# Performance work log

Measured on AMD Instinct MI355X. Metric: run time of the kernel, lower is better.

## Reference

```python
import jax, jax.numpy as jnp
import numpy as np

EMBED_DIM = 512
NUM_HEADS = 8
HEAD_DIM = EMBED_DIM // NUM_HEADS  # 64
KERNEL = 3  # spatial neighborhood kernel (time kernel is full t)
EPS = 1e-6


def _rms_norm(u, gamma):
    # RMSNorm over the last (head_dim) axis
    return u * jax.lax.rsqrt(jnp.mean(u * u, axis=-1, keepdims=True) + EPS) * gamma


def _apply_rotary(x, freqs):
    # x: (b, t, h, w, nh, hd); freqs: (t, h, w, hd//2) angles
    cos = jnp.cos(freqs)[None, :, :, :, None, :]
    sin = jnp.sin(freqs)[None, :, :, :, None, :]
    xe, xo = x[..., 0::2], x[..., 1::2]
    out = jnp.stack([xe * cos - xo * sin, xe * sin + xo * cos], axis=-1)
    return out.reshape(x.shape)


def setup_inputs() -> dict:
    key = jax.random.key(0)
    ks = jax.random.split(key, 6)
    b, t, h, w = 2, 8, 32, 32
    x = jax.random.normal(ks[0], (b, t, h, w, EMBED_DIM), dtype=jnp.float32)
    freqs = jax.random.normal(ks[1], (t, h, w, HEAD_DIM // 2), dtype=jnp.float32)
    w_in = jax.random.normal(ks[2], (3 * EMBED_DIM, EMBED_DIM), dtype=jnp.float32) * 0.02
    w_out = jax.random.normal(ks[3], (EMBED_DIM, EMBED_DIM), dtype=jnp.float32) * 0.02
    q_gamma = jnp.ones((HEAD_DIM,), dtype=jnp.float32)
    k_gamma = jnp.ones((HEAD_DIM,), dtype=jnp.float32)
    return {"x": x, "freqs": freqs, "w_in": w_in, "w_out": w_out,
            "q_gamma": q_gamma, "k_gamma": k_gamma}


def reference(x, freqs, w_in, w_out, q_gamma, k_gamma):
    b, t, H, W, c = x.shape
    nh, hd = NUM_HEADS, HEAD_DIM
    # fused QKV projection (torch Linear: y = x @ W^T)
    qkv = jnp.einsum('bthwc,oc->bthwo', x, w_in).reshape(b, t, H, W, nh, 3 * hd)
    q, k, v = jnp.split(qkv, 3, axis=-1)
    q = _apply_rotary(_rms_norm(q, q_gamma), freqs)
    k = _apply_rotary(_rms_norm(k, k_gamma), freqs)
    # NATTEN 3D neighborhood: full attention over time, 3x3 spatial window
    # clamped to stay inside the feature map (window shifts near borders).
    Kc = KERNEL // 2
    ih = jnp.clip(jnp.arange(H) - Kc, 0, H - KERNEL)[:, None] + jnp.arange(KERNEL)  # (H,3)
    iw = jnp.clip(jnp.arange(W) - Kc, 0, W - KERNEL)[:, None] + jnp.arange(KERNEL)  # (W,3)

    def window(u):
        # u: (b, t, H, W, nh, hd) -> (b, H, W, nh, t*K*K, hd)
        uw = jnp.take(jnp.take(u, ih, axis=2), iw, axis=4)  # (b,t,H,K,W,K,nh,hd)
        uw = jnp.transpose(uw, (0, 2, 4, 6, 1, 3, 5, 7))     # (b,H,W,nh,t,K,K,hd)
        return uw.reshape(b, H, W, nh, t * KERNEL * KERNEL, hd)

    k_win = window(k)
    v_win = window(v)
    scale = hd ** -0.5
    scores = jnp.einsum('bthwnd,bhwnkd->bhwntk', q, k_win) * scale
    attn = jax.nn.softmax(scores, axis=-1)
    out = jnp.einsum('bhwntk,bhwnkd->bthwnd', attn, v_win)
    out = out.reshape(b, t, H, W, nh * hd)
    return jnp.einsum('bthwc,oc->bthwo', out, w_out)
```

## Files before the change

### kernel.cpp

```cpp
#include <hip/hip_runtime.h>
#include <hip/hip_bf16.h>
#include <math.h>

#define NH 8
#define C_ 512
#define C3 1536
#define NTOK 16384

typedef __attribute__((ext_vector_type(8))) short short8;
typedef __attribute__((ext_vector_type(4))) float f32x4;
typedef __attribute__((address_space(3))) void* lds_ptr_t;
typedef const __attribute__((address_space(1))) void* gbl_ptr_t;

static __device__ __forceinline__ ushort f2bf(float f) {
  __hip_bfloat16 h = __float2bfloat16(f);
  return *reinterpret_cast<ushort*>(&h);
}
static __device__ __forceinline__ float bf2f(ushort u) {
  uint t = ((uint)u) << 16;
  float f;
  __builtin_memcpy(&f, &t, 4);
  return f;
}

__global__ __launch_bounds__(256) void cast3_kernel(
    const float* __restrict__ x, const float* __restrict__ wi,
    const float* __restrict__ wo, ushort* __restrict__ xb,
    ushort* __restrict__ wib, ushort* __restrict__ wob) {
  const int blk = blockIdx.x;
  const float* src;
  ushort* dst;
  int i;
  if (blk < 4096)      { src = x;  dst = xb;  i = blk * 256 + threadIdx.x; }
  else if (blk < 4480) { src = wi; dst = wib; i = (blk - 4096) * 256 + threadIdx.x; }
  else                 { src = wo; dst = wob; i = (blk - 4480) * 256 + threadIdx.x; }
  const float4* p = (const float4*)src + (size_t)i * 2;
  float4 v0 = p[0], v1 = p[1];
  union { ushort u[8]; uint4 v; } r;
  r.u[0] = f2bf(v0.x); r.u[1] = f2bf(v0.y); r.u[2] = f2bf(v0.z); r.u[3] = f2bf(v0.w);
  r.u[4] = f2bf(v1.x); r.u[5] = f2bf(v1.y); r.u[6] = f2bf(v1.z); r.u[7] = f2bf(v1.w);
  *(uint4*)(dst + (size_t)i * 8) = r.v;
}

#define TBM 128
#define TBN 128
#define TBK 32
#define TILE_U ((TBM + TBN) * TBK)

static __device__ __forceinline__ void stage_tile(
    const ushort* __restrict__ A, const ushort* __restrict__ B,
    ushort* As, ushort* Bs, int bm, int bn, int K, int k0, int tid) {
#pragma unroll
  for (int it = 0; it < 2; ++it) {
    int c = it * 256 + tid;
    int row = c >> 2;
    int sk = ((c & 3) ^ ((row >> 1) & 3)) * 8;
    __builtin_amdgcn_global_load_lds(
        (gbl_ptr_t)(const void*)(A + (size_t)(bm + row) * K + k0 + sk),
        (lds_ptr_t)(As + (size_t)c * 8), 16, 0, 0);
    __builtin_amdgcn_global_load_lds(
        (gbl_ptr_t)(const void*)(B + (size_t)(bn + row) * K + k0 + sk),
        (lds_ptr_t)(Bs + (size_t)c * 8), 16, 0, 0);
  }
}

template <bool BF16OUT>
__global__ __launch_bounds__(256) void gemm_bt_bf16(
    const ushort* __restrict__ A, const ushort* __restrict__ B,
    void* __restrict__ Cv, int N, int K, int GX) {
  __shared__ ushort smem[2 * TILE_U];
  const int tid  = threadIdx.x;
  const int wave = tid >> 6;
  const int lane = tid & 63;
  const int nwg = gridDim.x;
  const int wg = (blockIdx.x & 7) * (nwg >> 3) + (blockIdx.x >> 3);
  const int bm = (wg / GX) * TBM;
  const int bn = (wg % GX) * TBN;
  const int wr = (wave >> 1) * 64;
  const int wc = (wave & 1) * 64;
  const int lm = lane & 15;
  const int g4 = lane >> 4;

  f32x4 acc[4][4];
#pragma unroll
  for (int m = 0; m < 4; ++m)
#pragma unroll
    for (int n = 0; n < 4; ++n) acc[m][n] = (f32x4){0.f, 0.f, 0.f, 0.f};

  const int ko = (g4 ^ ((lm >> 1) & 3)) * 8;

  const int nt = K / TBK;
  stage_tile(A, B, smem, smem + TBM * TBK, bm, bn, K, 0, tid);
  __syncthreads();

  int cur = 0;
  for (int t = 0; t < nt; ++t) {
    if (t + 1 < nt) {
      ushort* Asn = smem + (cur ^ 1) * TILE_U;
      stage_tile(A, B, Asn, Asn + TBM * TBK, bm, bn, K, (t + 1) * TBK, tid);
    }
    const ushort* As = smem + cur * TILE_U;
    const ushort* Bs = As + TBM * TBK;
    short8 av[4], bv[4];
#pragma unroll
    for (int m = 0; m < 4; ++m)
      av[m] = *(const short8*)&As[(wr + m * 16 + lm) * TBK + ko];
#pragma unroll
    for (int n = 0; n < 4; ++n)
      bv[n] = *(const short8*)&Bs[(wc + n * 16 + lm) * TBK + ko];
#pragma unroll
    for (int m = 0; m < 4; ++m)
#pragma unroll
      for (int n = 0; n < 4; ++n)
        acc[m][n] = __builtin_amdgcn_mfma_f32_16x16x32_bf16(av[m], bv[n], acc[m][n], 0, 0, 0);
    __syncthreads();
    cur ^= 1;
  }

  const int cr = g4 * 4;
  const int cc = lm;

  if (BF16OUT) {
    ushort* Cs = smem;
    ushort* C = (ushort*)Cv;
#pragma unroll
    for (int h = 0; h < 2; ++h) {
      __syncthreads();
      if ((wave >> 1) == h) {
#pragma unroll
        for (int m = 0; m < 4; ++m)
#pragma unroll
          for (int n = 0; n < 4; ++n)
#pragma unroll
            for (int r = 0; r < 4; ++r)
              Cs[(m * 16 + cr + r) * 128 + wc + n * 16 + cc] = f2bf(acc[m][n][r]);
      }
      __syncthreads();
#pragma unroll
      for (int i = 0; i < 4; ++i) {
        int idx = i * 256 + tid;
        int row = idx >> 4, ch = idx & 15;
        uint4 v = *(const uint4*)&Cs[row * 128 + ch * 8];
        *(uint4*)(C + (size_t)(bm + h * 64 + row) * N + bn + ch * 8) = v;
      }
    }
  } else {
    float* Csf = (float*)smem;
    float* C = (float*)Cv;
#pragma unroll
    for (int s = 0; s < 4; ++s) {
      __syncthreads();
      if ((wave >> 1) == (s >> 1)) {
#pragma unroll
        for (int mi = 0; mi < 2; ++mi)
#pragma unroll
          for (int n = 0; n < 4; ++n)
#pragma unroll
            for (int r = 0; r < 4; ++r) {
              int m = (s & 1) * 2 + mi;
              Csf[(mi * 16 + cr + r) * 128 + wc + n * 16 + cc] = acc[m][n][r];
            }
      }
      __syncthreads();
#pragma unroll
      for (int i = 0; i < 4; ++i) {
        int idx = i * 256 + tid;
        int row = idx >> 5, ch = idx & 31;
        float4 v = *(const float4*)&Csf[row * 128 + ch * 4];
        *(float4*)(C + (size_t)(bm + s * 32 + row) * N + bn + ch * 4) = v;
      }
    }
  }
}

__global__ __launch_bounds__(256) void norm_rope_kernel(
    ushort* __restrict__ qkv, const float* __restrict__ freqs,
    const float* __restrict__ qg, const float* __restrict__ kg) {
  const int task = blockIdx.x * 4 + (threadIdx.x >> 6);
  const int L = threadIdx.x & 63;
  const int n = task & 7;
  const int m = task >> 3;
  const int w = m & 31, h = (m >> 5) & 31, t = (m >> 10) & 7;
  const int dp = L & 31;

  ushort* base = qkv + (size_t)m * C3 + n * 192;
  uint val = *(uint*)(base + 2 * L);
  float x0 = bf2f((ushort)(val & 0xffffu));
  float x1 = bf2f((ushort)(val >> 16));

  float ss = x0 * x0 + x1 * x1;
#pragma unroll
  for (int off = 16; off >= 1; off >>= 1) ss += __shfl_xor(ss, off, 32);
  const float r = rsqrtf(ss * (1.f / 64.f) + 1e-6f);
  const float* gp = (L < 32) ? qg : kg;
  const float xe = x0 * r * gp[2 * dp];
  const float xo = x1 * r * gp[2 * dp + 1];

  const float f = freqs[(((t * 32 + h) * 32 + w) * 32) + dp];
  const float c = cosf(f), s = sinf(f);
  ushort o0 = f2bf(xe * c - xo * s);
  ushort o1 = f2bf(xe * s + xo * c);
  *(uint*)(base + 2 * L) = (uint)o0 | ((uint)o1 << 16);
}

__global__ __launch_bounds__(256) void attn_kernel(
    const ushort* __restrict__ qkv, ushort* __restrict__ outb) {
  __shared__ ushort lds[24576];
  ushort* K_s  = lds;
  ushort* Vt_s = lds + 12288;
  ushort* P_s  = lds;
  ushort* O_s  = lds + 12288;

  const int tid = threadIdx.x;
  const int wave = tid >> 6;
  const int lane = tid & 63;
  const int lin = blockIdx.x;
  const int bid = (lin & 7) * 256 + (lin >> 3);
  const int tw = bid & 7, th = (bid >> 3) & 15, n = (bid >> 7) & 7, b = bid >> 10;
  const int hb = th * 2, wb = tw * 4;
  const int hb0 = max(hb - 1, 0), wb0 = max(wb - 1, 0);
  const int lm = lane & 15, g4 = lane >> 4;

  float4 vreg[6];
#pragma unroll
  for (int it = 0; it < 6; ++it) {
    int c = it * 256 + tid;
    int kr = c >> 3, gv = c & 7;
    int sc = kr >> 3, t = kr & 7;
    int kh = sc / 6, kw = sc - kh * 6;
    int hh = min(hb0 + kh, 31), ww = min(wb0 + kw, 31);
    size_t m = (((size_t)(b * 8 + t) * 32 + hh) * 32 + ww);
    vreg[it] = *(const float4*)(qkv + m * C3 + n * 192 + 128 + gv * 8);
  }

#pragma unroll
  for (int it = 0; it < 6; ++it) {
    int c = it * 256 + tid;
    int kr = c >> 3, g = (c & 7) ^ (kr & 7);
    int sc = kr >> 3, t = kr & 7;
    int kh = sc / 6, kw = sc - kh * 6;
    int hh = min(hb0 + kh, 31), ww = min(wb0 + kw, 31);
    size_t m = (((size_t)(b * 8 + t) * 32 + hh) * 32 + ww);
    const ushort* srcK = qkv + m * C3 + n * 192 + 64 + g * 8;
    ushort* dstK = K_s + (size_t)(it * 256 + wave * 64) * 8;
    __builtin_amdgcn_global_load_lds((gbl_ptr_t)(const void*)srcK, (lds_ptr_t)dstK, 16, 0, 0);
  }

  short8 bq[2];
  {
    int q = wave * 16 + lm;
    int tq = q >> 3, p = q & 7;
    size_t mq = (((size_t)(b * 8 + tq) * 32 + (hb + (p >> 2))) * 32 + (wb + (p & 3)));
    const ushort* qp = qkv + mq * C3 + n * 192;
#pragma unroll
    for (int kk = 0; kk < 2; ++kk)
      bq[kk] = *(const short8*)(qp + (kk * 4 + g4) * 8);
  }

  __syncthreads();

#pragma unroll
  for (int it = 0; it < 6; ++it) {
    int c = it * 256 + tid;
    int kr = c >> 3, gv = c & 7;
    int ck = kr >> 3, kin = kr & 7;
    union { float4 f; ushort u[8]; } vv;
    vv.f = vreg[it];
#pragma unroll
    for (int j = 0; j < 8; ++j) {
      int d = gv * 8 + j;
      int cks = ck ^ ((j ^ gv) & 7);
      Vt_s[d * 192 + cks * 8 + kin] = vv.u[j];
    }
  }

  f32x4 st[12];
#pragma unroll
  for (int kf = 0; kf < 12; ++kf) st[kf] = (f32x4){0.f, 0.f, 0.f, 0.f};
#pragma unroll
  for (int kk = 0; kk < 2; ++kk)
#pragma unroll
    for (int kf = 0; kf < 12; ++kf) {
      int kr = kf * 16 + lm;
      short8 a = *(const short8*)&K_s[kr * 64 + (((kk * 4 + g4) ^ (kr & 7)) * 8)];
      st[kf] = __builtin_amdgcn_mfma_f32_16x16x32_bf16(a, bq[kk], st[kf], 0, 0, 0);
    }

  const int p = lm & 7;
  const int qh = hb + (p >> 2), qw = wb + (p & 3);
  const int loh = min(max(qh - 1, 0), 29), low = min(max(qw - 1, 0), 29);
  uint mk = 0;
#pragma unroll
  for (int kf = 0; kf < 12; ++kf) {
    int sc = kf * 2 + (g4 >> 1);
    int kh = sc / 6, kw = sc - kh * 6;
    int khg = hb0 + kh, kwg = wb0 + kw;
    bool ok = (khg >= loh) && (khg <= loh + 2) && (kwg >= low) && (kwg <= low + 2);
    mk |= (uint)ok << kf;
  }
  const float scale = 0.125f;
#pragma unroll
  for (int kf = 0; kf < 12; ++kf) {
    bool ok = (mk >> kf) & 1;
#pragma unroll
    for (int r = 0; r < 4; ++r)
      st[kf][r] = ok ? st[kf][r] * scale : -1e30f;
  }
  float mx = -1e30f;
#pragma unroll
  for (int kf = 0; kf < 12; ++kf)
#pragma unroll
    for (int r = 0; r < 4; ++r) mx = fmaxf(mx, st[kf][r]);
  mx = fmaxf(mx, __shfl_xor(mx, 16));
  mx = fmaxf(mx, __shfl_xor(mx, 32));
  float s = 0.f;
#pragma unroll
  for (int kf = 0; kf < 12; ++kf)
#pragma unroll
    for (int r = 0; r < 4; ++r) {
      float e = __expf(st[kf][r] - mx);
      st[kf][r] = e;
      s += e;
    }
  s += __shfl_xor(s, 16);
  s += __shfl_xor(s, 32);
  const float inv = 1.f / s;
  __syncthreads();

  {
    const int q = wave * 16 + lm;
    ushort* Prow = P_s + q * 192 + (g4 & 1) * 4;
#pragma unroll
    for (int kf = 0; kf < 12; ++kf) {
      uint lo = (uint)f2bf(st[kf][0] * inv) | ((uint)f2bf(st[kf][1] * inv) << 16);
      uint hi = (uint)f2bf(st[kf][2] * inv) | ((uint)f2bf(st[kf][3] * inv) << 16);
      int ck = kf * 2 + (g4 >> 1);
      int cks = ck ^ (lm & 7);
      uint2 val; val.x = lo; val.y = hi;
      *(uint2*)(Prow + cks * 8) = val;
    }
  }
  __syncthreads();

  f32x4 ao0 = (f32x4){0.f, 0.f, 0.f, 0.f};
  f32x4 ao1 = (f32x4){0.f, 0.f, 0.f, 0.f};
  f32x4 ao2 = (f32x4){0.f, 0.f, 0.f, 0.f};
  f32x4 ao3 = (f32x4){0.f, 0.f, 0.f, 0.f};
  const int drow = wave * 16 + lm;
  const int dsw = (lm & 7) ^ ((wave * 2 + (lm >> 3)) & 7);
#pragma unroll
  for (int kk = 0; kk < 6; ++kk) {
    int ch = kk * 4 + g4;
    short8 bv = *(const short8*)&Vt_s[drow * 192 + ((ch ^ dsw) * 8)];
    int pch = (ch ^ (lm & 7)) * 8;
    short8 av0 = *(const short8*)&P_s[(0 * 16 + lm) * 192 + pch];
    short8 av1 = *(const short8*)&P_s[(1 * 16 + lm) * 192 + pch];
    short8 av2 = *(const short8*)&P_s[(2 * 16 + lm) * 192 + pch];
    short8 av3 = *(const short8*)&P_s[(3 * 16 + lm) * 192 + pch];
    ao0 = __builtin_amdgcn_mfma_f32_16x16x32_bf16(av0, bv, ao0, 0, 0, 0);
    ao1 = __builtin_amdgcn_mfma_f32_16x16x32_bf16(av1, bv, ao1, 0, 0, 0);
    ao2 = __builtin_amdgcn_mfma_f32_16x16x32_bf16(av2, bv, ao2, 0, 0, 0);
    ao3 = __builtin_amdgcn_mfma_f32_16x16x32_bf16(av3, bv, ao3, 0, 0, 0);
  }
  __syncthreads();

#pragma unroll
  for (int r = 0; r < 4; ++r) {
    O_s[(0 * 16 + g4 * 4 + r) * 68 + (wave * 16 + lm)] = f2bf(ao0[r]);
    O_s[(1 * 16 + g4 * 4 + r) * 68 + (wave * 16 + lm)] = f2bf(ao1[r]);
    O_s[(2 * 16 + g4 * 4 + r) * 68 + (wave * 16 + lm)] = f2bf(ao2[r]);
    O_s[(3 * 16 + g4 * 4 + r) * 68 + (wave * 16 + lm)] = f2bf(ao3[r]);
  }
  __syncthreads();
#pragma unroll
  for (int i = 0; i < 2; ++i) {
    int idx = i * 256 + tid;
    int q = idx >> 3, c = idx & 7;
    short8 v = *(const short8*)&O_s[q * 68 + c * 8];
    int tq = q >> 3, pp = q & 7;
    size_t m = (((size_t)(b * 8 + tq) * 32 + (hb + (pp >> 2))) * 32 + (wb + (pp & 3)));
    *(short8*)(outb + m * (size_t)C_ + n * 64 + c * 8) = v;
  }
}

extern "C" void kernel_launch(void* const* d_in, const int* in_sizes, int n_in,
                              void* d_out, int out_size, void* d_ws, size_t ws_size,
                              hipStream_t stream) {
  const float* x     = (const float*)d_in[0];
  const float* freqs = (const float*)d_in[1];
  const float* w_in  = (const float*)d_in[2];
  const float* w_out = (const float*)d_in[3];
  const float* qg    = (const float*)d_in[4];
  const float* kg    = (const float*)d_in[5];
  float* out = (float*)d_out;

  char* ws = (char*)d_ws;
  ushort* qkv   = (ushort*)ws;
  ushort* xb    = (ushort*)(ws + (size_t)NTOK * C3 * 2);
  ushort* wib   = xb + (size_t)NTOK * C_;
  ushort* wob   = wib + (size_t)C3 * C_;
  ushort* attnb = wob + (size_t)C_ * C_;

  cast3_kernel<<<4608, 256, 0, stream>>>(x, w_in, w_out, xb, wib, wob);

  gemm_bt_bf16<true><<<1536, 256, 0, stream>>>(xb, wib, qkv, C3, C_, 12);
  norm_rope_kernel<<<(NTOK * NH) / 4, 256, 0, stream>>>(qkv, freqs, qg, kg);
  attn_kernel<<<2048, 256, 0, stream>>>(qkv, attnb);
  gemm_bt_bf16<false><<<512, 256, 0, stream>>>(attnb, wob, out, C_, C_, 4);
}
```

Baseline: 107.7 us.

## Replace QKV GEMM with 256x256-tile 8-wave phased pipelined kernel

Adds a new bf16 GEMM for the QKV projection that uses 256x256 output tiles, 512 threads, a BK of 64 and double-buffered LDS filled by direct global-to-LDS loads. Each K step is split into four phases, with prefetch of the next tile interleaved between MFMA batches and explicit vmcnt waits and barriers. The output is written back through LDS with coalesced stores, and workgroups are remapped across XCDs. The goal is more data reuse and better overlap of loads with MFMA work. The cost is a grid of only 384 blocks of 128KB LDS each, which may leave compute units underused.

```diff
diff --git a/kernel.cpp b/kernel.cpp
--- a/kernel.cpp
+++ b/kernel.cpp
@@ -22,6 +22,9 @@
   __builtin_memcpy(&f, &t, 4);
   return f;
 }
+
+#define GLD16(src, dst) \
+  __builtin_amdgcn_global_load_lds((gbl_ptr_t)(const void*)(src), (lds_ptr_t)(dst), 16, 0, 0)
 
 __global__ __launch_bounds__(256) void cast3_kernel(
     const float* __restrict__ x, const float* __restrict__ wi,
@@ -42,6 +45,125 @@
   *(uint4*)(dst + (size_t)i * 8) = r.v;
 }
 
+__global__ __launch_bounds__(512, 2) void gemm256_8ph_bf16(
+    const ushort* __restrict__ A, const ushort* __restrict__ B,
+    ushort* __restrict__ C, int N, int K, int GX) {
+  __shared__ ushort smem[65536];
+  const int tid  = threadIdx.x;
+  const int wave = tid >> 6;
+  const int lane = tid & 63;
+  const int lm = lane & 15, g4 = lane >> 4;
+  const int wm = wave >> 2, wn = wave & 3;
+  const int nwg = gridDim.x;
+  const int wg = (blockIdx.x & 7) * (nwg >> 3) + (blockIdx.x >> 3);
+  const int bm = (wg / GX) * 256;
+  const int bn = (wg % GX) * 256;
+
+  const int trow = tid >> 3;
+  const int slot8 = ((tid & 7) ^ (trow & 7)) * 8;
+  const ushort* Arow = A + (size_t)(bm + trow) * K + slot8;
+  const ushort* Brow = B + (size_t)(bn + trow) * K + slot8;
+  const size_t sstr = (size_t)64 * K;
+  ushort* ldsT = smem + tid * 8;
+
+  const int nt = K >> 6;
+
+  f32x4 acc[8][4];
+#pragma unroll
+  for (int m = 0; m < 8; ++m)
+#pragma unroll
+    for (int n = 0; n < 4; ++n) acc[m][n] = (f32x4){0.f, 0.f, 0.f, 0.f};
+
+  GLD16(Arow + 0 * sstr, ldsT + 0);
+  GLD16(Arow + 2 * sstr, ldsT + 8192);
+  GLD16(Brow + 0 * sstr, ldsT + 16384);
+  GLD16(Brow + 1 * sstr, ldsT + 20480);
+  GLD16(Brow + 2 * sstr, ldsT + 24576);
+  GLD16(Brow + 3 * sstr, ldsT + 28672);
+  GLD16(Arow + 1 * sstr, ldsT + 4096);
+  GLD16(Arow + 3 * sstr, ldsT + 12288);
+  asm volatile("s_waitcnt vmcnt(2)" ::: "memory");
+  __builtin_amdgcn_s_barrier();
+  asm volatile("" ::: "memory");
+
+  int cur = 0;
+  for (int t = 0; t < nt; ++t) {
+    const ushort* As = smem + cur * 32768;
+    const ushort* Bs = As + 16384;
+    ushort* Ln = smem + (cur ^ 1) * 32768 + tid * 8;
+    const ushort* An = Arow + (size_t)(t + 1) * 64;
+    const ushort* Bn = Brow + (size_t)(t + 1) * 64;
+    const bool st = (t + 1 < nt);
+    short8 a[4][2], bb[2][2];
+#pragma unroll
+    for (int p = 0; p < 4; ++p) {
+      const int qm = p >> 1, qn = p & 1;
+      if ((p & 1) == 0) {
+#pragma unroll
+        for (int mf = 0; mf < 4; ++mf)
+#pragma unroll
+          for (int kk = 0; kk < 2; ++kk) {
+            const int row = wm * 128 + qm * 64 + mf * 16 + lm;
+            a[mf][kk] = *(const short8*)&As[row * 64 + (((kk * 4 + g4) ^ (lm & 7)) * 8)];
+          }
+      }
+#pragma unroll
+      for (int nf = 0; nf < 2; ++nf)
+#pragma unroll
+        for (int kk = 0; kk < 2; ++kk) {
+          const int row = wn * 64 + qn * 32 + nf * 16 + lm;
+          bb[nf][kk] = *(const short8*)&Bs[row * 64 + (((kk * 4 + g4) ^ (lm & 7)) * 8)];
+        }
+      if (st) {
+        if (p == 0) { GLD16(An + 0 * sstr, Ln + 0);     GLD16(An + 2 * sstr, Ln + 8192);  }
+        if (p == 1) { GLD16(Bn + 0 * sstr, Ln + 16384); GLD16(Bn + 1 * sstr, Ln + 20480); }
+        if (p == 2) { GLD16(Bn + 2 * sstr, Ln + 24576); GLD16(Bn + 3 * sstr, Ln + 28672); }
+        if (p == 3) { GLD16(An + 1 * sstr, Ln + 4096);  GLD16(An + 3 * sstr, Ln + 12288); }
+      }
+      __builtin_amdgcn_s_barrier();
+      asm volatile("s_waitcnt lgkmcnt(0)" ::: "memory");
+      __builtin_amdgcn_s_setprio(1);
+#pragma unroll
+      for (int mf = 0; mf < 4; ++mf)
+#pragma unroll
+        for (int nf = 0; nf < 2; ++nf)
+#pragma unroll
+          for (int kk = 0; kk < 2; ++kk)
+            acc[qm * 4 + mf][qn * 2 + nf] = __builtin_amdgcn_mfma_f32_16x16x32_bf16(
+                a[mf][kk], bb[nf][kk], acc[qm * 4 + mf][qn * 2 + nf], 0, 0, 0);
+      __builtin_amdgcn_s_setprio(0);
+      if (p == 1) {
+        if (st) asm volatile("s_waitcnt vmcnt(4)" ::: "memory");
+        else    asm volatile("s_waitcnt vmcnt(0)" ::: "memory");
+      }
+      if (p == 3 && st)
+        asm volatile("s_waitcnt vmcnt(2)" ::: "memory");
+      __builtin_amdgcn_s_barrier();
+      asm volatile("" ::: "memory");
+    }
+    cur ^= 1;
+  }
+
+  __syncthreads();
+  ushort* Cs = smem;
+#pragma unroll
+  for (int mf = 0; mf < 8; ++mf)
+#pragma unroll
+    for (int nf = 0; nf < 4; ++nf)
+#pragma unroll
+      for (int r = 0; r < 4; ++r)
+        Cs[(wm * 128 + mf * 16 + g4 * 4 + r) * 256 + wn * 64 + nf * 16 + lm] =
+            f2bf(acc[mf][nf][r]);
+  __syncthreads();
+#pragma unroll
+  for (int i = 0; i < 16; ++i) {
+    const int idx = i * 512 + tid;
+    const int row = idx >> 5, ch = idx & 31;
+    uint4 v = *(const uint4*)&Cs[row * 256 + ch * 8];
+    *(uint4*)(C + (size_t)(bm + row) * N + bn + ch * 8) = v;
+  }
+}
+
 #define TBM 128
 #define TBN 128
 #define TBK 32
@@ -403,7 +525,7 @@
 
   cast3_kernel<<<4608, 256, 0, stream>>>(x, w_in, w_out, xb, wib, wob);
 
-  gemm_bt_bf16<true><<<1536, 256, 0, stream>>>(xb, wib, qkv, C3, C_, 12);
+  gemm256_8ph_bf16<<<384, 512, 0, stream>>>(xb, wib, qkv, C3, C_, 6);
   norm_rope_kernel<<<(NTOK * NH) / 4, 256, 0, stream>>>(qkv, freqs, qg, kg);
   attn_kernel<<<2048, 256, 0, stream>>>(qkv, attnb);
   gemm_bt_bf16<false><<<512, 256, 0, stream>>>(attnb, wob, out, C_, C_, 4);
```

Measured after the change: 115.1 us. 6.9% more time.

## Fuse RMSNorm and rotary embedding into QKV GEMM epilogue, precompute cos/sin

Applied to the files above, without the earlier changes.

Removes the separate norm_rope kernel and applies RMSNorm plus rotary embedding in the QKV GEMM epilogue, working on a bf16 tile staged in LDS. The cast kernel gains extra blocks that precompute cos/sin of the frequencies into a scratch buffer that aliases the attention-output workspace. This saves one kernel launch and a full read-modify-write pass over the q and k parts of the QKV tensor. In exchange the GEMM epilogue does more work, including per-element cos/sin loads, and a 128-wide tile only covers one 64-wide q/k/v segment per half-row group, so correctness depends on bn alignment with the 192-column head layout.

```diff
diff --git a/kernel.cpp b/kernel.cpp
--- a/kernel.cpp
+++ b/kernel.cpp
@@ -25,9 +25,25 @@
 
 __global__ __launch_bounds__(256) void cast3_kernel(
     const float* __restrict__ x, const float* __restrict__ wi,
-    const float* __restrict__ wo, ushort* __restrict__ xb,
-    ushort* __restrict__ wib, ushort* __restrict__ wob) {
+    const float* __restrict__ wo, const float* __restrict__ fr,
+    ushort* __restrict__ xb, ushort* __restrict__ wib,
+    ushort* __restrict__ wob, float2* __restrict__ csn) {
   const int blk = blockIdx.x;
+  if (blk >= 4608) {
+    int i = (blk - 4608) * 256 + threadIdx.x;
+    const float4* fp = (const float4*)fr + (size_t)i * 2;
+    float4 a = fp[0], b = fp[1];
+    float v[8] = {a.x, a.y, a.z, a.w, b.x, b.y, b.z, b.w};
+    float2 o[8];
+#pragma unroll
+    for (int j = 0; j < 8; ++j) { o[j].x = cosf(v[j]); o[j].y = sinf(v[j]); }
+    float4* op = (float4*)(csn + (size_t)i * 8);
+    op[0] = make_float4(o[0].x, o[0].y, o[1].x, o[1].y);
+    op[1] = make_float4(o[2].x, o[2].y, o[3].x, o[3].y);
+    op[2] = make_float4(o[4].x, o[4].y, o[5].x, o[5].y);
+    op[3] = make_float4(o[6].x, o[6].y, o[7].x, o[7].y);
+    return;
+  }
   const float* src;
   ushort* dst;
   int i;
@@ -61,6 +77,117 @@
     __builtin_amdgcn_global_load_lds(
         (gbl_ptr_t)(const void*)(B + (size_t)(bn + row) * K + k0 + sk),
         (lds_ptr_t)(Bs + (size_t)c * 8), 16, 0, 0);
+  }
+}
+
+#define CSTR 136
+
+__global__ __launch_bounds__(256) void gemm_qkv_fused(
+    const ushort* __restrict__ A, const ushort* __restrict__ B,
+    ushort* __restrict__ C, int N, int K, int GX,
+    const float2* __restrict__ csn, const float* __restrict__ qg,
+    const float* __restrict__ kg) {
+  __shared__ ushort smem[2 * TILE_U];
+  __shared__ float gsh[128];
+  const int tid  = threadIdx.x;
+  const int wave = tid >> 6;
+  const int lane = tid & 63;
+  const int nwg = gridDim.x;
+  const int wg = (blockIdx.x & 7) * (nwg >> 3) + (blockIdx.x >> 3);
+  const int bm = (wg / GX) * TBM;
+  const int bn = (wg % GX) * TBN;
+  const int wr = (wave >> 1) * 64;
+  const int wc = (wave & 1) * 64;
+  const int lm = lane & 15;
+  const int g4 = lane >> 4;
+
+  if (tid < 128) gsh[tid] = (tid < 64) ? qg[tid] : kg[tid - 64];
+
+  f32x4 acc[4][4];
+#pragma unroll
+  for (int m = 0; m < 4; ++m)
+#pragma unroll
+    for (int n = 0; n < 4; ++n) acc[m][n] = (f32x4){0.f, 0.f, 0.f, 0.f};
+
+  const int ko = (g4 ^ ((lm >> 1) & 3)) * 8;
+
+  const int nt = K / TBK;
+  stage_tile(A, B, smem, smem + TBM * TBK, bm, bn, K, 0, tid);
+  __syncthreads();
+
+  int cur = 0;
+  for (int t = 0; t < nt; ++t) {
+    if (t + 1 < nt) {
+      ushort* Asn = smem + (cur ^ 1) * TILE_U;
+      stage_tile(A, B, Asn, Asn + TBM * TBK, bm, bn, K, (t + 1) * TBK, tid);
+    }
+    const ushort* As = smem + cur * TILE_U;
+    const ushort* Bs = As + TBM * TBK;
+    short8 av[4], bv[4];
+#pragma unroll
+    for (int m = 0; m < 4; ++m)
+      av[m] = *(const short8*)&As[(wr + m * 16 + lm) * TBK + ko];
+#pragma unroll
+    for (int n = 0; n < 4; ++n)
+      bv[n] = *(const short8*)&Bs[(wc + n * 16 + lm) * TBK + ko];
+#pragma unroll
+    for (int m = 0; m < 4; ++m)
+#pragma unroll
+      for (int n = 0; n < 4; ++n)
+        acc[m][n] = __builtin_amdgcn_mfma_f32_16x16x32_bf16(av[m], bv[n], acc[m][n], 0, 0, 0);
+    __syncthreads();
+    cur ^= 1;
+  }
+
+  const int cr = g4 * 4;
+  const int cc = lm;
+  ushort* Cs = smem;
+  const int row_e = tid >> 2;
+  const int cg    = (tid >> 1) & 1;
+  const int half  = tid & 1;
+  const int colg  = bn + cg * 64;
+  const int type  = (colg % 192) >> 6;
+  const int gofs  = (type & 1) * 64;
+
+#pragma unroll
+  for (int h = 0; h < 2; ++h) {
+    __syncthreads();
+    if ((wave >> 1) == h) {
+#pragma unroll
+      for (int m = 0; m < 4; ++m)
+#pragma unroll
+        for (int n = 0; n < 4; ++n)
+#pragma unroll
+          for (int r = 0; r < 4; ++r)
+            Cs[(m * 16 + cr + r) * CSTR + wc + n * 16 + cc] = f2bf(acc[m][n][r]);
+    }
+    __syncthreads();
+    union { uint4 q[4]; ushort u[32]; } L;
+    {
+      const uint4* srcp = (const uint4*)&Cs[row_e * CSTR + cg * 64 + half * 32];
+      L.q[0] = srcp[0]; L.q[1] = srcp[1]; L.q[2] = srcp[2]; L.q[3] = srcp[3];
+    }
+    const int tokm = bm + h * 64 + row_e;
+    float f[32], ss = 0.f;
+#pragma unroll
+    for (int j = 0; j < 32; ++j) { f[j] = bf2f(L.u[j]); ss += f[j] * f[j]; }
+    ss += __shfl_xor(ss, 1);
+    const float rn = rsqrtf(ss * (1.f / 64.f) + 1e-6f);
+    const int tloc = (tokm >> 10) & 7;
+    const float2* cb = csn + (((size_t)((tloc << 10) | (tokm & 1023))) << 5) + half * 16;
+    union { uint4 q[4]; ushort u[32]; } O;
+#pragma unroll
+    for (int dj = 0; dj < 16; ++dj) {
+      float2 cs2 = cb[dj];
+      float2 gg = *(const float2*)&gsh[gofs + (half * 16 + dj) * 2];
+      float xe = f[2 * dj]     * rn * gg.x;
+      float xo = f[2 * dj + 1] * rn * gg.y;
+      O.u[2 * dj]     = f2bf(xe * cs2.x - xo * cs2.y);
+      O.u[2 * dj + 1] = f2bf(xe * cs2.y + xo * cs2.x);
+    }
+    if (type == 2) { O.q[0] = L.q[0]; O.q[1] = L.q[1]; O.q[2] = L.q[2]; O.q[3] = L.q[3]; }
+    uint4* dst = (uint4*)(C + (size_t)tokm * N + colg + half * 32);
+    dst[0] = O.q[0]; dst[1] = O.q[1]; dst[2] = O.q[2]; dst[3] = O.q[3];
   }
 }
 
@@ -173,36 +300,6 @@
   }
 }
 
-__global__ __launch_bounds__(256) void norm_rope_kernel(
-    ushort* __restrict__ qkv, const float* __restrict__ freqs,
-    const float* __restrict__ qg, const float* __restrict__ kg) {
-  const int task = blockIdx.x * 4 + (threadIdx.x >> 6);
-  const int L = threadIdx.x & 63;
-  const int n = task & 7;
-  const int m = task >> 3;
-  const int w = m & 31, h = (m >> 5) & 31, t = (m >> 10) & 7;
-  const int dp = L & 31;
-
-  ushort* base = qkv + (size_t)m * C3 + n * 192;
-  uint val = *(uint*)(base + 2 * L);
-  float x0 = bf2f((ushort)(val & 0xffffu));
-  float x1 = bf2f((ushort)(val >> 16));
-
-  float ss = x0 * x0 + x1 * x1;
-#pragma unroll
-  for (int off = 16; off >= 1; off >>= 1) ss += __shfl_xor(ss, off, 32);
-  const float r = rsqrtf(ss * (1.f / 64.f) + 1e-6f);
-  const float* gp = (L < 32) ? qg : kg;
-  const float xe = x0 * r * gp[2 * dp];
-  const float xo = x1 * r * gp[2 * dp + 1];
-
-  const float f = freqs[(((t * 32 + h) * 32 + w) * 32) + dp];
-  const float c = cosf(f), s = sinf(f);
-  ushort o0 = f2bf(xe * c - xo * s);
-  ushort o1 = f2bf(xe * s + xo * c);
-  *(uint*)(base + 2 * L) = (uint)o0 | ((uint)o1 << 16);
-}
-
 __global__ __launch_bounds__(256) void attn_kernel(
     const ushort* __restrict__ qkv, ushort* __restrict__ outb) {
   __shared__ ushort lds[24576];
@@ -400,11 +497,11 @@
   ushort* wib   = xb + (size_t)NTOK * C_;
   ushort* wob   = wib + (size_t)C3 * C_;
   ushort* attnb = wob + (size_t)C_ * C_;
-
-  cast3_kernel<<<4608, 256, 0, stream>>>(x, w_in, w_out, xb, wib, wob);
-
-  gemm_bt_bf16<true><<<1536, 256, 0, stream>>>(xb, wib, qkv, C3, C_, 12);
-  norm_rope_kernel<<<(NTOK * NH) / 4, 256, 0, stream>>>(qkv, freqs, qg, kg);
+  float2* csn = (float2*)attnb;
+
+  cast3_kernel<<<4736, 256, 0, stream>>>(x, w_in, w_out, freqs, xb, wib, wob, csn);
+
+  gemm_qkv_fused<<<1536, 256, 0, stream>>>(xb, wib, qkv, C3, C_, 12, csn, qg, kg);
   attn_kernel<<<2048, 256, 0, stream>>>(qkv, attnb);
   gemm_bt_bf16<false><<<512, 256, 0, stream>>>(attnb, wob, out, C_, C_, 4);
 }
```

Measured after the change: 132.4 us. 1.23x slower.

## Fuse RMSNorm and rotary into attention kernel, precompute cos/sin table

Applied to the files above, without the earlier changes.

Removes the separate norm_rope kernel. RMSNorm and rotary embedding for Q and K are now applied inside the attention kernel as it loads them. The cos/sin table is precomputed by extra blocks of the cast kernel and stored temporarily in the output buffer, which the final GEMM overwrites later. This saves a full read-modify-write pass over Q and K and one kernel launch. In exchange, K is recomputed about 4.5 times per token (overlapping windows), the direct global-to-LDS load for K is lost, and register pressure goes up.

```diff
diff --git a/kernel.cpp b/kernel.cpp
--- a/kernel.cpp
+++ b/kernel.cpp
@@ -25,9 +25,25 @@
 
 __global__ __launch_bounds__(256) void cast3_kernel(
     const float* __restrict__ x, const float* __restrict__ wi,
-    const float* __restrict__ wo, ushort* __restrict__ xb,
-    ushort* __restrict__ wib, ushort* __restrict__ wob) {
+    const float* __restrict__ wo, const float* __restrict__ fr,
+    ushort* __restrict__ xb, ushort* __restrict__ wib,
+    ushort* __restrict__ wob, float2* __restrict__ csn) {
   const int blk = blockIdx.x;
+  if (blk >= 4608) {
+    int i = (blk - 4608) * 256 + threadIdx.x;
+    const float4* fp = (const float4*)fr + (size_t)i * 2;
+    float4 a = fp[0], b = fp[1];
+    float v[8] = {a.x, a.y, a.z, a.w, b.x, b.y, b.z, b.w};
+    float2 o[8];
+#pragma unroll
+    for (int j = 0; j < 8; ++j) { o[j].x = cosf(v[j]); o[j].y = sinf(v[j]); }
+    float4* op = (float4*)(csn + (size_t)i * 8);
+    op[0] = make_float4(o[0].x, o[0].y, o[1].x, o[1].y);
+    op[1] = make_float4(o[2].x, o[2].y, o[3].x, o[3].y);
+    op[2] = make_float4(o[4].x, o[4].y, o[5].x, o[5].y);
+    op[3] = make_float4(o[6].x, o[6].y, o[7].x, o[7].y);
+    return;
+  }
   const float* src;
   ushort* dst;
   int i;
@@ -173,38 +189,10 @@
   }
 }
 
-__global__ __launch_bounds__(256) void norm_rope_kernel(
-    ushort* __restrict__ qkv, const float* __restrict__ freqs,
-    const float* __restrict__ qg, const float* __restrict__ kg) {
-  const int task = blockIdx.x * 4 + (threadIdx.x >> 6);
-  const int L = threadIdx.x & 63;
-  const int n = task & 7;
-  const int m = task >> 3;
-  const int w = m & 31, h = (m >> 5) & 31, t = (m >> 10) & 7;
-  const int dp = L & 31;
-
-  ushort* base = qkv + (size_t)m * C3 + n * 192;
-  uint val = *(uint*)(base + 2 * L);
-  float x0 = bf2f((ushort)(val & 0xffffu));
-  float x1 = bf2f((ushort)(val >> 16));
-
-  float ss = x0 * x0 + x1 * x1;
-#pragma unroll
-  for (int off = 16; off >= 1; off >>= 1) ss += __shfl_xor(ss, off, 32);
-  const float r = rsqrtf(ss * (1.f / 64.f) + 1e-6f);
-  const float* gp = (L < 32) ? qg : kg;
-  const float xe = x0 * r * gp[2 * dp];
-  const float xo = x1 * r * gp[2 * dp + 1];
-
-  const float f = freqs[(((t * 32 + h) * 32 + w) * 32) + dp];
-  const float c = cosf(f), s = sinf(f);
-  ushort o0 = f2bf(xe * c - xo * s);
-  ushort o1 = f2bf(xe * s + xo * c);
-  *(uint*)(base + 2 * L) = (uint)o0 | ((uint)o1 << 16);
-}
-
 __global__ __launch_bounds__(256) void attn_kernel(
-    const ushort* __restrict__ qkv, ushort* __restrict__ outb) {
+    const ushort* __restrict__ qkv, ushort* __restrict__ outb,
+    const float* __restrict__ csn, const float* __restrict__ qg,
+    const float* __restrict__ kg) {
   __shared__ ushort lds[24576];
   ushort* K_s  = lds;
   ushort* Vt_s = lds + 12288;
@@ -221,7 +209,8 @@
   const int hb0 = max(hb - 1, 0), wb0 = max(wb - 1, 0);
   const int lm = lane & 15, g4 = lane >> 4;
 
-  float4 vreg[6];
+  float4 vreg[6], kreg[6];
+  int mi6[6];
 #pragma unroll
   for (int it = 0; it < 6; ++it) {
     int c = it * 256 + tid;
@@ -230,20 +219,10 @@
     int kh = sc / 6, kw = sc - kh * 6;
     int hh = min(hb0 + kh, 31), ww = min(wb0 + kw, 31);
     size_t m = (((size_t)(b * 8 + t) * 32 + hh) * 32 + ww);
-    vreg[it] = *(const float4*)(qkv + m * C3 + n * 192 + 128 + gv * 8);
-  }
-
-#pragma unroll
-  for (int it = 0; it < 6; ++it) {
-    int c = it * 256 + tid;
-    int kr = c >> 3, g = (c & 7) ^ (kr & 7);
-    int sc = kr >> 3, t = kr & 7;
-    int kh = sc / 6, kw = sc - kh * 6;
-    int hh = min(hb0 + kh, 31), ww = min(wb0 + kw, 31);
-    size_t m = (((size_t)(b * 8 + t) * 32 + hh) * 32 + ww);
-    const ushort* srcK = qkv + m * C3 + n * 192 + 64 + g * 8;
-    ushort* dstK = K_s + (size_t)(it * 256 + wave * 64) * 8;
-    __builtin_amdgcn_global_load_lds((gbl_ptr_t)(const void*)srcK, (lds_ptr_t)dstK, 16, 0, 0);
+    mi6[it] = (int)(m & 8191);
+    const ushort* bp = qkv + m * C3 + n * 192;
+    vreg[it] = *(const float4*)(bp + 128 + gv * 8);
+    kreg[it] = *(const float4*)(bp + 64 + gv * 8);
   }
 
   short8 bq[2];
@@ -252,9 +231,72 @@
     int tq = q >> 3, p = q & 7;
     size_t mq = (((size_t)(b * 8 + tq) * 32 + (hb + (p >> 2))) * 32 + (wb + (p & 3)));
     const ushort* qp = qkv + mq * C3 + n * 192;
-#pragma unroll
-    for (int kk = 0; kk < 2; ++kk)
-      bq[kk] = *(const short8*)(qp + (kk * 4 + g4) * 8);
+    union { short8 s; ushort u[8]; } Lq0, Lq1;
+    Lq0.s = *(const short8*)(qp + g4 * 8);
+    Lq1.s = *(const short8*)(qp + (4 + g4) * 8);
+    float fq[16];
+    float ssq = 0.f;
+#pragma unroll
+    for (int j = 0; j < 8; ++j) { fq[j] = bf2f(Lq0.u[j]); ssq += fq[j] * fq[j]; }
+#pragma unroll
+    for (int j = 0; j < 8; ++j) { fq[8 + j] = bf2f(Lq1.u[j]); ssq += fq[8 + j] * fq[8 + j]; }
+    ssq += __shfl_xor(ssq, 16);
+    ssq += __shfl_xor(ssq, 32);
+    const float rq = rsqrtf(ssq * (1.f / 64.f) + 1e-6f);
+    const int miq = (int)(mq & 8191);
+#pragma unroll
+    for (int kk = 0; kk < 2; ++kk) {
+      const int ch0 = (kk * 4 + g4) * 8;
+      const float4 ga = *(const float4*)(qg + ch0);
+      const float4 gb = *(const float4*)(qg + ch0 + 4);
+      const float* cbp = csn + (size_t)miq * 64 + ch0;
+      const float4 c0 = *(const float4*)cbp;
+      const float4 c1 = *(const float4*)(cbp + 4);
+      const float* fv = &fq[kk * 8];
+      union { short8 s; ushort u[8]; } O;
+      float xe, xo;
+      xe = fv[0] * rq * ga.x; xo = fv[1] * rq * ga.y;
+      O.u[0] = f2bf(xe * c0.x - xo * c0.y); O.u[1] = f2bf(xe * c0.y + xo * c0.x);
+      xe = fv[2] * rq * ga.z; xo = fv[3] * rq * ga.w;
+      O.u[2] = f2bf(xe * c0.z - xo * c0.w); O.u[3] = f2bf(xe * c0.w + xo * c0.z);
+      xe = fv[4] * rq * gb.x; xo = fv[5] * rq * gb.y;
+      O.u[4] = f2bf(xe * c1.x - xo * c1.y); O.u[5] = f2bf(xe * c1.y + xo * c1.x);
+      xe = fv[6] * rq * gb.z; xo = fv[7] * rq * gb.w;
+      O.u[6] = f2bf(xe * c1.z - xo * c1.w); O.u[7] = f2bf(xe * c1.w + xo * c1.z);
+      bq[kk] = O.s;
+    }
+  }
+
+#pragma unroll
+  for (int it = 0; it < 6; ++it) {
+    int c = it * 256 + tid;
+    int kr = c >> 3, g = c & 7;
+    union { float4 f; ushort u[8]; } L;
+    L.f = kreg[it];
+    float f0 = bf2f(L.u[0]), f1 = bf2f(L.u[1]), f2 = bf2f(L.u[2]), f3 = bf2f(L.u[3]);
+    float f4 = bf2f(L.u[4]), f5 = bf2f(L.u[5]), f6 = bf2f(L.u[6]), f7 = bf2f(L.u[7]);
+    float ss = f0 * f0 + f1 * f1 + f2 * f2 + f3 * f3 +
+               f4 * f4 + f5 * f5 + f6 * f6 + f7 * f7;
+    ss += __shfl_xor(ss, 1);
+    ss += __shfl_xor(ss, 2);
+    ss += __shfl_xor(ss, 4);
+    const float rn = rsqrtf(ss * (1.f / 64.f) + 1e-6f);
+    const float4 ga = *(const float4*)(kg + g * 8);
+    const float4 gb = *(const float4*)(kg + g * 8 + 4);
+    const float* cbp = csn + (size_t)mi6[it] * 64 + g * 8;
+    const float4 c0 = *(const float4*)cbp;
+    const float4 c1 = *(const float4*)(cbp + 4);
+    union { short8 s; ushort u[8]; } O;
+    float xe, xo;
+    xe = f0 * rn * ga.x; xo = f1 * rn * ga.y;
+    O.u[0] = f2bf(xe * c0.x - xo * c0.y); O.u[1] = f2bf(xe * c0.y + xo * c0.x);
+    xe = f2 * rn * ga.z; xo = f3 * rn * ga.w;
+    O.u[2] = f2bf(xe * c0.z - xo * c0.w); O.u[3] = f2bf(xe * c0.w + xo * c0.z);
+    xe = f4 * rn * gb.x; xo = f5 * rn * gb.y;
+    O.u[4] = f2bf(xe * c1.x - xo * c1.y); O.u[5] = f2bf(xe * c1.y + xo * c1.x);
+    xe = f6 * rn * gb.z; xo = f7 * rn * gb.w;
+    O.u[6] = f2bf(xe * c1.z - xo * c1.w); O.u[7] = f2bf(xe * c1.w + xo * c1.z);
+    *(short8*)&K_s[kr * 64 + ((g ^ (kr & 7)) * 8)] = O.s;
   }
 
   __syncthreads();
@@ -400,11 +442,12 @@
   ushort* wib   = xb + (size_t)NTOK * C_;
   ushort* wob   = wib + (size_t)C3 * C_;
   ushort* attnb = wob + (size_t)C_ * C_;
-
-  cast3_kernel<<<4608, 256, 0, stream>>>(x, w_in, w_out, xb, wib, wob);
+  float* csn = out;
+
+  cast3_kernel<<<4736, 256, 0, stream>>>(x, w_in, w_out, freqs, xb, wib, wob,
+                                         (float2*)csn);
 
   gemm_bt_bf16<true><<<1536, 256, 0, stream>>>(xb, wib, qkv, C3, C_, 12);
-  norm_rope_kernel<<<(NTOK * NH) / 4, 256, 0, stream>>>(qkv, freqs, qg, kg);
-  attn_kernel<<<2048, 256, 0, stream>>>(qkv, attnb);
+  attn_kernel<<<2048, 256, 0, stream>>>(qkv, attnb, csn, qg, kg);
   gemm_bt_bf16<false><<<512, 256, 0, stream>>>(attnb, wob, out, C_, C_, 4);
 }
```

Result: faster. 100.9 us (-6.4%).
